# Kernel tuning notes

Hardware: AMD Instinct MI355X
Metric: run time of the kernel (lower is better)

The kernel has to match this reference:

```python
import jax, jax.numpy as jnp
import numpy as np

B, L, D, Q, H = 16, 2048, 1024, 1024, 256
NEG_NUM = -10000.0


def setup_inputs() -> dict:
    key = jax.random.key(0)
    ks = jax.random.split(key, 8)
    ctx = jax.random.normal(ks[0], (B, L, D), dtype=jnp.float32)
    query = jax.random.normal(ks[1], (B, Q), dtype=jnp.float32)
    mask = jax.random.randint(ks[2], (B, L), 0, 2, dtype=jnp.int32)
    # lin_in2proj: Linear(D+Q, H)
    lim1 = 1.0 / np.sqrt(D + Q)
    W1 = jax.random.uniform(ks[3], (H, D + Q), jnp.float32, -lim1, lim1)
    b1 = jax.random.uniform(ks[4], (H,), jnp.float32, -lim1, lim1)
    # lin_proj2score: weight_norm(Linear(H, 1)), dim=0 -> g scalar per row
    lim2 = 1.0 / np.sqrt(H)
    v = jax.random.uniform(ks[5], (1, H), jnp.float32, -lim2, lim2)
    g = jnp.linalg.norm(v).reshape(1, 1)  # weight_norm init: g = ||v||
    b2 = jax.random.uniform(ks[6], (1,), jnp.float32, -lim2, lim2)
    return {"ctx": ctx, "query": query, "mask": mask,
            "W1": W1, "b1": b1, "v": v, "g": g, "b2": b2}


def reference(ctx, query, mask, W1, b1, v, g, b2):
    d = ctx.shape[-1]
    # concat([ctx, query_expanded]) @ W1^T == ctx @ W1c^T + query @ W1q^T
    Wc, Wq = W1[:, :d], W1[:, d:]
    hid = jnp.tanh(jnp.einsum('bld,hd->blh', ctx, Wc)
                   + jnp.einsum('bq,hq->bh', query, Wq)[:, None, :]
                   + b1)                                 # (B, L, H)
    w2 = (g * v / jnp.linalg.norm(v))[0]                 # weight-normed row (H,)
    score = jnp.einsum('blh,h->bl', hid, w2) + b2[0]     # (B, L)
    score = jnp.where(mask == 1, NEG_NUM, score)
    p_ctx = jax.nn.softmax(score, axis=-1)               # (B, L)
    expected_ctx = jnp.einsum('bl,bld->bd', p_ctx, ctx)  # (B, D)
    return expected_ctx, p_ctx
```

## Files before the change

### kernel.cpp

```cpp
#include <hip/hip_runtime.h>
#include <hip/hip_bf16.h>

#define BB 16
#define LCTX 2048
#define DDIM 1024
#define QDIM 1024
#define HDIM 256
#define NEGV -10000.0f

typedef __attribute__((ext_vector_type(8))) short short8;
typedef __attribute__((ext_vector_type(4))) float f32x4;

__device__ inline unsigned short f2bf(float x) {
    unsigned int u = __float_as_uint(x);
    unsigned int r = (u + 0x7fffu + ((u >> 16) & 1u)) >> 16;
    return (unsigned short)r;
}

__global__ __launch_bounds__(256) void k_prep(const float* __restrict__ query,
                                              const float* __restrict__ W1,
                                              const float* __restrict__ b1,
                                              const float* __restrict__ v,
                                              const float* __restrict__ g,
                                              float* __restrict__ qproj,
                                              unsigned short* __restrict__ Wc_sw,
                                              float* __restrict__ w2) {
    int bid = blockIdx.x;
    if (bid < 1024) {
        int b = bid >> 6;
        int hq = bid & 63;
        int wid = threadIdx.x >> 6, lane = threadIdx.x & 63;
        int h = hq * 4 + wid;
        const float* q = query + b * QDIM;
        const float* w = W1 + (size_t)h * (DDIM + QDIM) + DDIM;
        float s = 0.f;
        #pragma unroll 4
        for (int k = lane; k < QDIM; k += 64) s += q[k] * w[k];
        #pragma unroll
        for (int o = 32; o; o >>= 1) s += __shfl_down(s, o);
        if (lane == 0) qproj[b * HDIM + h] = s + b1[h];
    } else if (bid < 1280) {
        int h = bid - 1024;
        const float* src = W1 + (size_t)h * (DDIM + QDIM);
        int hx = h & 7;
        for (int d = threadIdx.x; d < DDIM; d += 256) {
            int kt = d >> 6;
            int s  = (d >> 3) & 7;
            int dl = d & 7;
            int dp = (kt << 6) + ((s ^ hx) << 3) + dl;
            Wc_sw[h * DDIM + dp] = f2bf(src[d]);
        }
    } else {
        __shared__ float red[256];
        float vv = (threadIdx.x < HDIM) ? v[threadIdx.x] : 0.f;
        red[threadIdx.x] = vv * vv;
        __syncthreads();
        for (int o = 128; o; o >>= 1) {
            if (threadIdx.x < o) red[threadIdx.x] += red[threadIdx.x + o];
            __syncthreads();
        }
        float nrm = sqrtf(red[0]);
        if (threadIdx.x < HDIM) w2[threadIdx.x] = g[0] * vv / nrm;
    }
}

__global__ __launch_bounds__(256, 3) void k_score(const float* __restrict__ ctx,
                                                  const unsigned short* __restrict__ Wc_sw,
                                                  const float* __restrict__ qproj,
                                                  const float* __restrict__ w2,
                                                  const float* __restrict__ b2,
                                                  const int* __restrict__ mask,
                                                  float* __restrict__ e_ws,
                                                  float* __restrict__ esum_ws,
                                                  float* __restrict__ part) {
    __shared__ unsigned short At[64 * 64];
    __shared__ unsigned short Wt[256 * 64];
    int tid = threadIdx.x;
    int wid = tid >> 6, lane = tid & 63;
    int hl = lane & 15, lhi = lane >> 4;
    int bid = blockIdx.x;
    int row0 = bid * 64;
    int b = row0 >> 11;

    float qp[4], wv[4];
    #pragma unroll
    for (int ht = 0; ht < 4; ht++) {
        int h = wid * 64 + ht * 16 + hl;
        qp[ht] = qproj[b * HDIM + h];
        wv[ht] = w2[h];
    }

    f32x4 acc[4][4];
    #pragma unroll
    for (int mt = 0; mt < 4; mt++)
        #pragma unroll
        for (int ht = 0; ht < 4; ht++)
            acc[mt][ht] = (f32x4){0.f, 0.f, 0.f, 0.f};

    int srow = tid >> 2;
    int scol = (tid & 3) * 16;
    const float* csrc = ctx + (size_t)(row0 + srow) * DDIM + scol;
    int c0 = (tid & 3) * 2;
    int sx = srow & 7;

    for (int kt = 0; kt < 16; kt++) {
        #pragma unroll
        for (int i = 0; i < 8; i++) {
            int n = i * 256 + tid;
            const unsigned short* gsrc = Wc_sw + (size_t)(n >> 3) * DDIM + kt * 64 + (n & 7) * 8;
            __builtin_amdgcn_global_load_lds(
                (const __attribute__((address_space(1))) unsigned int*)gsrc,
                (__attribute__((address_space(3))) unsigned int*)(Wt + (i * 256 + (tid & ~63)) * 8),
                16, 0, 0);
        }
        const float* cp = csrc + kt * 64;
        float4 cv0 = *(const float4*)(cp + 0);
        float4 cv1 = *(const float4*)(cp + 4);
        float4 cv2 = *(const float4*)(cp + 8);
        float4 cv3 = *(const float4*)(cp + 12);
        short8 p0 = { (short)f2bf(cv0.x), (short)f2bf(cv0.y), (short)f2bf(cv0.z), (short)f2bf(cv0.w),
                      (short)f2bf(cv1.x), (short)f2bf(cv1.y), (short)f2bf(cv1.z), (short)f2bf(cv1.w) };
        short8 p1 = { (short)f2bf(cv2.x), (short)f2bf(cv2.y), (short)f2bf(cv2.z), (short)f2bf(cv2.w),
                      (short)f2bf(cv3.x), (short)f2bf(cv3.y), (short)f2bf(cv3.z), (short)f2bf(cv3.w) };
        *(short8*)(At + srow * 64 + (((c0 + 0) ^ sx) << 3)) = p0;
        *(short8*)(At + srow * 64 + (((c0 + 1) ^ sx) << 3)) = p1;
        __syncthreads();

        #pragma unroll
        for (int ks = 0; ks < 2; ks++) {
            int s = ks * 4 + lhi;
            short8 af[4], bfr[4];
            #pragma unroll
            for (int mt = 0; mt < 4; mt++) {
                int m = mt * 16 + hl;
                af[mt] = *(const short8*)(At + m * 64 + ((s ^ (m & 7)) << 3));
            }
            #pragma unroll
            for (int ht = 0; ht < 4; ht++) {
                int h = wid * 64 + ht * 16 + hl;
                bfr[ht] = *(const short8*)(Wt + h * 64 + ((s ^ (h & 7)) << 3));
            }
            #pragma unroll
            for (int mt = 0; mt < 4; mt++)
                #pragma unroll
                for (int ht = 0; ht < 4; ht++)
                    acc[mt][ht] = __builtin_amdgcn_mfma_f32_16x16x32_bf16(af[mt], bfr[ht], acc[mt][ht], 0, 0, 0);
        }
        __syncthreads();
    }

    float* sb  = (float*)At;
    float* sbe = sb + 256;
    #pragma unroll
    for (int mt = 0; mt < 4; mt++) {
        #pragma unroll
        for (int r = 0; r < 4; r++) {
            float partial = 0.f;
            #pragma unroll
            for (int ht = 0; ht < 4; ht++) {
                float x = acc[mt][ht][r] + qp[ht];
                x = fminf(fmaxf(x, -15.f), 15.f);
                float e = __expf(2.f * x);
                partial += (e - 1.f) / (e + 1.f) * wv[ht];
            }
            #pragma unroll
            for (int o = 1; o < 16; o <<= 1) partial += __shfl_xor(partial, o);
            if (hl == 0) sb[wid * 64 + mt * 16 + lhi * 4 + r] = partial;
        }
    }
    __syncthreads();

    if (tid < 64) {
        float s = sb[tid] + sb[64 + tid] + sb[128 + tid] + sb[192 + tid] + b2[0];
        int grow = row0 + tid;
        int bb = grow >> 11, ll = grow & 2047;
        float e = (mask[bb * 2048 + ll] == 1) ? 0.f : __expf(s);
        e_ws[grow] = e;
        sbe[tid] = e;
        float tot = e;
        #pragma unroll
        for (int o = 32; o; o >>= 1) tot += __shfl_down(tot, o);
        if (tid == 0) esum_ws[bid] = tot;
    }
    __syncthreads();

    {
        int d0 = tid * 4;
        const float* cb = ctx + (size_t)row0 * DDIM + d0;
        float4 a = {0.f, 0.f, 0.f, 0.f};
        #pragma unroll 8
        for (int l = 0; l < 64; l++) {
            float el = sbe[l];
            float4 c = *(const float4*)(cb + (size_t)l * DDIM);
            a.x += el * c.x; a.y += el * c.y; a.z += el * c.z; a.w += el * c.w;
        }
        *(float4*)(part + (size_t)bid * DDIM + d0) = a;
    }
}

__global__ __launch_bounds__(256) void k_norm(const float* __restrict__ e_ws,
                                              const float* __restrict__ esum_ws,
                                              const float* __restrict__ part,
                                              float* __restrict__ out_exp,
                                              float* __restrict__ out_p) {
    int b = blockIdx.x, dc = blockIdx.y;
    int tid = threadIdx.x;
    float se = 0.f;
    #pragma unroll
    for (int j = 0; j < 32; j++) se += esum_ws[b * 32 + j];
    float inv = 1.f / se;
    if (tid < 128) {
        int d = dc * 128 + tid;
        float s = 0.f;
        #pragma unroll
        for (int j = 0; j < 32; j++) s += part[(size_t)(b * 32 + j) * DDIM + d];
        out_exp[b * DDIM + d] = s * inv;
    }
    int l = dc * 256 + tid;
    out_p[b * LCTX + l] = e_ws[b * LCTX + l] * inv;
}

extern "C" void kernel_launch(void* const* d_in, const int* in_sizes, int n_in,
                              void* d_out, int out_size, void* d_ws, size_t ws_size,
                              hipStream_t stream) {
    const float* ctx   = (const float*)d_in[0];
    const float* query = (const float*)d_in[1];
    const int*   mask  = (const int*)d_in[2];
    const float* W1    = (const float*)d_in[3];
    const float* b1    = (const float*)d_in[4];
    const float* v     = (const float*)d_in[5];
    const float* g     = (const float*)d_in[6];
    const float* b2    = (const float*)d_in[7];
    float* out_exp = (float*)d_out;
    float* out_p   = (float*)d_out + 16384;

    char* ws = (char*)d_ws;
    unsigned short* Wc_sw = (unsigned short*)ws;
    float* qproj = (float*)(ws + 524288);
    float* w2    = (float*)(ws + 540672);
    float* e_ws  = (float*)(ws + 541696);
    float* esum  = (float*)(ws + 672768);
    float* part  = (float*)(ws + 674816);

    k_prep <<<dim3(1281),   256, 0, stream>>>(query, W1, b1, v, g, qproj, Wc_sw, w2);
    k_score<<<dim3(512),    256, 0, stream>>>(ctx, Wc_sw, qproj, w2, b2, mask, e_ws, esum, part);
    k_norm <<<dim3(16, 8),  256, 0, stream>>>(e_ws, esum, part, out_exp, out_p);
}
```

Baseline: 59.15 us.

## Double-buffer W and ctx tiles with manual waitcnt software pipeline in k_score

Measured after the change: 59.87 us. Within noise of the previous version (+1.2%).

```diff
diff --git a/kernel.cpp b/kernel.cpp
--- a/kernel.cpp
+++ b/kernel.cpp
@@ -64,7 +64,7 @@
     }
 }
 
-__global__ __launch_bounds__(256, 3) void k_score(const float* __restrict__ ctx,
+__global__ __launch_bounds__(256, 2) void k_score(const float* __restrict__ ctx,
                                                   const unsigned short* __restrict__ Wc_sw,
                                                   const float* __restrict__ qproj,
                                                   const float* __restrict__ w2,
@@ -73,82 +73,125 @@
                                                   float* __restrict__ e_ws,
                                                   float* __restrict__ esum_ws,
                                                   float* __restrict__ part) {
-    __shared__ unsigned short At[64 * 64];
-    __shared__ unsigned short Wt[256 * 64];
+    __shared__ unsigned short Wt[2][256 * 64];
+    __shared__ unsigned short At[2][64 * 64];
     int tid = threadIdx.x;
     int wid = tid >> 6, lane = tid & 63;
     int hl = lane & 15, lhi = lane >> 4;
     int bid = blockIdx.x;
     int row0 = bid * 64;
     int b = row0 >> 11;
+    int wrow0 = wid * 64;
+
+    f32x4 acc[4][4];
+    #pragma unroll
+    for (int mt = 0; mt < 4; mt++)
+        #pragma unroll
+        for (int ht = 0; ht < 4; ht++)
+            acc[mt][ht] = (f32x4){0.f, 0.f, 0.f, 0.f};
+
+    int srow = tid >> 2;
+    int c0 = (tid & 3) * 2;
+    int sx = srow & 7;
+    const float* csrc = ctx + (size_t)(row0 + srow) * DDIM + (tid & 3) * 16;
+
+    float4 a0, a1, a2, a3, b0, b1, b2v, b3;
+
+#define STAGE_W(BUF, KT) do { \
+    _Pragma("unroll") \
+    for (int i_ = 0; i_ < 8; i_++) { \
+        const unsigned short* gsrc_ = Wc_sw + (size_t)(wrow0 + i_ * 8 + (lane >> 3)) * DDIM + (KT) * 64 + (lane & 7) * 8; \
+        __builtin_amdgcn_global_load_lds( \
+            (const __attribute__((address_space(1))) unsigned int*)gsrc_, \
+            (__attribute__((address_space(3))) unsigned int*)(&Wt[BUF][(wrow0 + i_ * 8) * 64]), \
+            16, 0, 0); \
+    } } while (0)
+
+#define CTX_ISSUE(KT, R0, R1, R2, R3) do { \
+    const float* cp_ = csrc + (KT) * 64; \
+    R0 = *(const float4*)(cp_ + 0);  R1 = *(const float4*)(cp_ + 4); \
+    R2 = *(const float4*)(cp_ + 8);  R3 = *(const float4*)(cp_ + 12); } while (0)
+
+#define WRITE_A(BUF, U0, U1, U2, U3) do { \
+    short8 p0_ = { (short)f2bf(U0.x), (short)f2bf(U0.y), (short)f2bf(U0.z), (short)f2bf(U0.w), \
+                   (short)f2bf(U1.x), (short)f2bf(U1.y), (short)f2bf(U1.z), (short)f2bf(U1.w) }; \
+    short8 p1_ = { (short)f2bf(U2.x), (short)f2bf(U2.y), (short)f2bf(U2.z), (short)f2bf(U2.w), \
+                   (short)f2bf(U3.x), (short)f2bf(U3.y), (short)f2bf(U3.z), (short)f2bf(U3.w) }; \
+    *(short8*)(&At[BUF][srow * 64 + (((c0 + 0) ^ sx) << 3)]) = p0_; \
+    *(short8*)(&At[BUF][srow * 64 + (((c0 + 1) ^ sx) << 3)]) = p1_; } while (0)
+
+#define COMPUTE(BUF) do { \
+    __builtin_amdgcn_s_setprio(1); \
+    _Pragma("unroll") \
+    for (int ks_ = 0; ks_ < 2; ks_++) { \
+        int s_ = ks_ * 4 + lhi; \
+        int xc_ = (s_ ^ (hl & 7)) << 3; \
+        short8 af_[4], bf_[4]; \
+        _Pragma("unroll") \
+        for (int mt_ = 0; mt_ < 4; mt_++) \
+            af_[mt_] = *(const short8*)(&At[BUF][(mt_ * 16 + hl) * 64 + xc_]); \
+        _Pragma("unroll") \
+        for (int ht_ = 0; ht_ < 4; ht_++) \
+            bf_[ht_] = *(const short8*)(&Wt[BUF][(wrow0 + ht_ * 16 + hl) * 64 + xc_]); \
+        _Pragma("unroll") \
+        for (int mt_ = 0; mt_ < 4; mt_++) \
+            _Pragma("unroll") \
+            for (int ht_ = 0; ht_ < 4; ht_++) \
+                acc[mt_][ht_] = __builtin_amdgcn_mfma_f32_16x16x32_bf16(af_[mt_], bf_[ht_], acc[mt_][ht_], 0, 0, 0); \
+    } \
+    __builtin_amdgcn_s_setprio(0); } while (0)
+
+#define BODY(T, R0, R1, R2, R3, U0, U1, U2, U3) do { \
+    STAGE_W(((T) + 1) & 1, ((T) + 1) & 15); \
+    __builtin_amdgcn_sched_barrier(0); \
+    CTX_ISSUE(((T) + 2) & 15, R0, R1, R2, R3); \
+    __builtin_amdgcn_sched_barrier(0); \
+    asm volatile("s_waitcnt vmcnt(16)" ::: "memory"); \
+    __builtin_amdgcn_sched_barrier(0); \
+    COMPUTE((T) & 1); \
+    asm volatile("s_waitcnt vmcnt(12)" ::: "memory"); \
+    __builtin_amdgcn_sched_barrier(0); \
+    WRITE_A(((T) + 1) & 1, U0, U1, U2, U3); \
+    asm volatile("s_waitcnt lgkmcnt(0)" ::: "memory"); \
+    __builtin_amdgcn_s_barrier(); \
+    __builtin_amdgcn_sched_barrier(0); } while (0)
+
+    CTX_ISSUE(0, a0, a1, a2, a3);
+    __builtin_amdgcn_sched_barrier(0);
+    STAGE_W(0, 0);
+    __builtin_amdgcn_sched_barrier(0);
+    asm volatile("s_waitcnt vmcnt(8)" ::: "memory");
+    __builtin_amdgcn_sched_barrier(0);
+    WRITE_A(0, a0, a1, a2, a3);
+    CTX_ISSUE(1, b0, b1, b2v, b3);
+    asm volatile("s_waitcnt lgkmcnt(0)" ::: "memory");
+    __builtin_amdgcn_s_barrier();
+    __builtin_amdgcn_sched_barrier(0);
+
+    BODY(0,  a0, a1, a2, a3,  b0, b1, b2v, b3);
+    BODY(1,  b0, b1, b2v, b3, a0, a1, a2, a3);
+    BODY(2,  a0, a1, a2, a3,  b0, b1, b2v, b3);
+    BODY(3,  b0, b1, b2v, b3, a0, a1, a2, a3);
+    BODY(4,  a0, a1, a2, a3,  b0, b1, b2v, b3);
+    BODY(5,  b0, b1, b2v, b3, a0, a1, a2, a3);
+    BODY(6,  a0, a1, a2, a3,  b0, b1, b2v, b3);
+    BODY(7,  b0, b1, b2v, b3, a0, a1, a2, a3);
+    BODY(8,  a0, a1, a2, a3,  b0, b1, b2v, b3);
+    BODY(9,  b0, b1, b2v, b3, a0, a1, a2, a3);
+    BODY(10, a0, a1, a2, a3,  b0, b1, b2v, b3);
+    BODY(11, b0, b1, b2v, b3, a0, a1, a2, a3);
+    BODY(12, a0, a1, a2, a3,  b0, b1, b2v, b3);
+    BODY(13, b0, b1, b2v, b3, a0, a1, a2, a3);
+    BODY(14, a0, a1, a2, a3,  b0, b1, b2v, b3);
+    BODY(15, b0, b1, b2v, b3, a0, a1, a2, a3);
 
     float qp[4], wv[4];
     #pragma unroll
     for (int ht = 0; ht < 4; ht++) {
-        int h = wid * 64 + ht * 16 + hl;
+        int h = wrow0 + ht * 16 + hl;
         qp[ht] = qproj[b * HDIM + h];
         wv[ht] = w2[h];
     }
-
-    f32x4 acc[4][4];
-    #pragma unroll
-    for (int mt = 0; mt < 4; mt++)
-        #pragma unroll
-        for (int ht = 0; ht < 4; ht++)
-            acc[mt][ht] = (f32x4){0.f, 0.f, 0.f, 0.f};
-
-    int srow = tid >> 2;
-    int scol = (tid & 3) * 16;
-    const float* csrc = ctx + (size_t)(row0 + srow) * DDIM + scol;
-    int c0 = (tid & 3) * 2;
-    int sx = srow & 7;
-
-    for (int kt = 0; kt < 16; kt++) {
-        #pragma unroll
-        for (int i = 0; i < 8; i++) {
-            int n = i * 256 + tid;
-            const unsigned short* gsrc = Wc_sw + (size_t)(n >> 3) * DDIM + kt * 64 + (n & 7) * 8;
-            __builtin_amdgcn_global_load_lds(
-                (const __attribute__((address_space(1))) unsigned int*)gsrc,
-                (__attribute__((address_space(3))) unsigned int*)(Wt + (i * 256 + (tid & ~63)) * 8),
-                16, 0, 0);
-        }
-        const float* cp = csrc + kt * 64;
-        float4 cv0 = *(const float4*)(cp + 0);
-        float4 cv1 = *(const float4*)(cp + 4);
-        float4 cv2 = *(const float4*)(cp + 8);
-        float4 cv3 = *(const float4*)(cp + 12);
-        short8 p0 = { (short)f2bf(cv0.x), (short)f2bf(cv0.y), (short)f2bf(cv0.z), (short)f2bf(cv0.w),
-                      (short)f2bf(cv1.x), (short)f2bf(cv1.y), (short)f2bf(cv1.z), (short)f2bf(cv1.w) };
-        short8 p1 = { (short)f2bf(cv2.x), (short)f2bf(cv2.y), (short)f2bf(cv2.z), (short)f2bf(cv2.w),
-                      (short)f2bf(cv3.x), (short)f2bf(cv3.y), (short)f2bf(cv3.z), (short)f2bf(cv3.w) };
-        *(short8*)(At + srow * 64 + (((c0 + 0) ^ sx) << 3)) = p0;
-        *(short8*)(At + srow * 64 + (((c0 + 1) ^ sx) << 3)) = p1;
-        __syncthreads();
-
-        #pragma unroll
-        for (int ks = 0; ks < 2; ks++) {
-            int s = ks * 4 + lhi;
-            short8 af[4], bfr[4];
-            #pragma unroll
-            for (int mt = 0; mt < 4; mt++) {
-                int m = mt * 16 + hl;
-                af[mt] = *(const short8*)(At + m * 64 + ((s ^ (m & 7)) << 3));
-            }
-            #pragma unroll
-            for (int ht = 0; ht < 4; ht++) {
-                int h = wid * 64 + ht * 16 + hl;
-                bfr[ht] = *(const short8*)(Wt + h * 64 + ((s ^ (h & 7)) << 3));
-            }
-            #pragma unroll
-            for (int mt = 0; mt < 4; mt++)
-                #pragma unroll
-                for (int ht = 0; ht < 4; ht++)
-                    acc[mt][ht] = __builtin_amdgcn_mfma_f32_16x16x32_bf16(af[mt], bfr[ht], acc[mt][ht], 0, 0, 0);
-        }
-        __syncthreads();
-    }
-
     float* sb  = (float*)At;
     float* sbe = sb + 256;
     #pragma unroll
@@ -191,8 +234,8 @@
         #pragma unroll 8
         for (int l = 0; l < 64; l++) {
             float el = sbe[l];
-            float4 c = *(const float4*)(cb + (size_t)l * DDIM);
-            a.x += el * c.x; a.y += el * c.y; a.z += el * c.z; a.w += el * c.w;
+            float4 cc = *(const float4*)(cb + (size_t)l * DDIM);
+            a.x += el * cc.x; a.y += el * cc.y; a.z += el * cc.z; a.w += el * cc.w;
         }
         *(float4*)(part + (size_t)bid * DDIM + d0) = a;
     }
```

## Double-buffer ctx staging, read weights from global, split weighted sum into kernel

Applied to the files above, without the earlier changes.

New measurement: 90.73 us. +53.4%, slower.

```diff
diff --git a/kernel.cpp b/kernel.cpp
--- a/kernel.cpp
+++ b/kernel.cpp
@@ -6,7 +6,6 @@
 #define DDIM 1024
 #define QDIM 1024
 #define HDIM 256
-#define NEGV -10000.0f
 
 typedef __attribute__((ext_vector_type(8))) short short8;
 typedef __attribute__((ext_vector_type(4))) float f32x4;
@@ -23,7 +22,7 @@
                                               const float* __restrict__ v,
                                               const float* __restrict__ g,
                                               float* __restrict__ qproj,
-                                              unsigned short* __restrict__ Wc_sw,
+                                              unsigned short* __restrict__ Wc_kmaj,
                                               float* __restrict__ w2) {
     int bid = blockIdx.x;
     if (bid < 1024) {
@@ -42,13 +41,11 @@
     } else if (bid < 1280) {
         int h = bid - 1024;
         const float* src = W1 + (size_t)h * (DDIM + QDIM);
-        int hx = h & 7;
         for (int d = threadIdx.x; d < DDIM; d += 256) {
             int kt = d >> 6;
-            int s  = (d >> 3) & 7;
-            int dl = d & 7;
-            int dp = (kt << 6) + ((s ^ hx) << 3) + dl;
-            Wc_sw[h * DDIM + dp] = f2bf(src[d]);
+            int oct = (d >> 3) & 7;
+            int j = d & 7;
+            Wc_kmaj[(size_t)kt * 16384 + h * 64 + oct * 8 + j] = f2bf(src[d]);
         }
     } else {
         __shared__ float red[256];
@@ -64,23 +61,83 @@
     }
 }
 
-__global__ __launch_bounds__(256, 3) void k_score(const float* __restrict__ ctx,
-                                                  const unsigned short* __restrict__ Wc_sw,
+__global__ __launch_bounds__(256, 2) void k_score(const float* __restrict__ ctx,
+                                                  const unsigned short* __restrict__ Wc_kmaj,
                                                   const float* __restrict__ qproj,
                                                   const float* __restrict__ w2,
-                                                  const float* __restrict__ b2,
+                                                  const float* __restrict__ b2p,
                                                   const int* __restrict__ mask,
                                                   float* __restrict__ e_ws,
-                                                  float* __restrict__ esum_ws,
-                                                  float* __restrict__ part) {
-    __shared__ unsigned short At[64 * 64];
-    __shared__ unsigned short Wt[256 * 64];
+                                                  float* __restrict__ esum_ws) {
+    __shared__ unsigned short At[2][64 * 256];
     int tid = threadIdx.x;
     int wid = tid >> 6, lane = tid & 63;
     int hl = lane & 15, lhi = lane >> 4;
-    int bid = blockIdx.x;
-    int row0 = bid * 64;
+    int row0 = blockIdx.x * 64;
     int b = row0 >> 11;
+
+    f32x4 acc[4][4];
+    #pragma unroll
+    for (int mt = 0; mt < 4; mt++)
+        #pragma unroll
+        for (int ht = 0; ht < 4; ht++)
+            acc[mt][ht] = (f32x4){0.f, 0.f, 0.f, 0.f};
+
+    int srow = tid >> 2;
+    int q = tid & 3;
+    int sxr = srow & 7;
+    const float* csrc = ctx + (size_t)(row0 + srow) * DDIM + q * 64;
+
+#define STAGE(BUF, G) do { \
+    const float* sp_ = csrc + (G) * 256; \
+    _Pragma("unroll") \
+    for (int bat_ = 0; bat_ < 4; bat_++) { \
+        float4 v0_ = *(const float4*)(sp_ + bat_ * 16 + 0); \
+        float4 v1_ = *(const float4*)(sp_ + bat_ * 16 + 4); \
+        float4 v2_ = *(const float4*)(sp_ + bat_ * 16 + 8); \
+        float4 v3_ = *(const float4*)(sp_ + bat_ * 16 + 12); \
+        short8 h0_ = { (short)f2bf(v0_.x), (short)f2bf(v0_.y), (short)f2bf(v0_.z), (short)f2bf(v0_.w), \
+                       (short)f2bf(v1_.x), (short)f2bf(v1_.y), (short)f2bf(v1_.z), (short)f2bf(v1_.w) }; \
+        short8 h1_ = { (short)f2bf(v2_.x), (short)f2bf(v2_.y), (short)f2bf(v2_.z), (short)f2bf(v2_.w), \
+                       (short)f2bf(v3_.x), (short)f2bf(v3_.y), (short)f2bf(v3_.z), (short)f2bf(v3_.w) }; \
+        int o0_ = (q * 8 + bat_ * 2 + 0) ^ sxr; \
+        int o1_ = (q * 8 + bat_ * 2 + 1) ^ sxr; \
+        *(short8*)(&At[BUF][srow * 256 + o0_ * 8]) = h0_; \
+        *(short8*)(&At[BUF][srow * 256 + o1_ * 8]) = h1_; \
+    } } while (0)
+
+#define COMPUTE(BUF, G) do { \
+    _Pragma("unroll") \
+    for (int kt_ = 0; kt_ < 4; kt_++) { \
+        int ktg_ = (G) * 4 + kt_; \
+        _Pragma("unroll") \
+        for (int ks_ = 0; ks_ < 2; ks_++) { \
+            int sl_ = kt_ * 8 + ks_ * 4 + lhi; \
+            short8 af_[4], bf_[4]; \
+            _Pragma("unroll") \
+            for (int mt_ = 0; mt_ < 4; mt_++) { \
+                int m_ = mt_ * 16 + hl; \
+                af_[mt_] = *(const short8*)(&At[BUF][m_ * 256 + (sl_ ^ (m_ & 7)) * 8]); \
+            } \
+            _Pragma("unroll") \
+            for (int ht_ = 0; ht_ < 4; ht_++) { \
+                int h_ = wid * 64 + ht_ * 16 + hl; \
+                bf_[ht_] = *(const short8*)(Wc_kmaj + (size_t)ktg_ * 16384 + h_ * 64 + (ks_ * 4 + lhi) * 8); \
+            } \
+            _Pragma("unroll") \
+            for (int mt_ = 0; mt_ < 4; mt_++) \
+                _Pragma("unroll") \
+                for (int ht_ = 0; ht_ < 4; ht_++) \
+                    acc[mt_][ht_] = __builtin_amdgcn_mfma_f32_16x16x32_bf16(af_[mt_], bf_[ht_], acc[mt_][ht_], 0, 0, 0); \
+        } } } while (0)
+
+    STAGE(0, 0);
+    __syncthreads();
+    COMPUTE(0, 0); STAGE(1, 1); __syncthreads();
+    COMPUTE(1, 1); STAGE(0, 2); __syncthreads();
+    COMPUTE(0, 2); STAGE(1, 3); __syncthreads();
+    COMPUTE(1, 3);
+    __syncthreads();
 
     float qp[4], wv[4];
     #pragma unroll
@@ -89,66 +146,6 @@
         qp[ht] = qproj[b * HDIM + h];
         wv[ht] = w2[h];
     }
-
-    f32x4 acc[4][4];
-    #pragma unroll
-    for (int mt = 0; mt < 4; mt++)
-        #pragma unroll
-        for (int ht = 0; ht < 4; ht++)
-            acc[mt][ht] = (f32x4){0.f, 0.f, 0.f, 0.f};
-
-    int srow = tid >> 2;
-    int scol = (tid & 3) * 16;
-    const float* csrc = ctx + (size_t)(row0 + srow) * DDIM + scol;
-    int c0 = (tid & 3) * 2;
-    int sx = srow & 7;
-
-    for (int kt = 0; kt < 16; kt++) {
-        #pragma unroll
-        for (int i = 0; i < 8; i++) {
-            int n = i * 256 + tid;
-            const unsigned short* gsrc = Wc_sw + (size_t)(n >> 3) * DDIM + kt * 64 + (n & 7) * 8;
-            __builtin_amdgcn_global_load_lds(
-                (const __attribute__((address_space(1))) unsigned int*)gsrc,
-                (__attribute__((address_space(3))) unsigned int*)(Wt + (i * 256 + (tid & ~63)) * 8),
-                16, 0, 0);
-        }
-        const float* cp = csrc + kt * 64;
-        float4 cv0 = *(const float4*)(cp + 0);
-        float4 cv1 = *(const float4*)(cp + 4);
-        float4 cv2 = *(const float4*)(cp + 8);
-        float4 cv3 = *(const float4*)(cp + 12);
-        short8 p0 = { (short)f2bf(cv0.x), (short)f2bf(cv0.y), (short)f2bf(cv0.z), (short)f2bf(cv0.w),
-                      (short)f2bf(cv1.x), (short)f2bf(cv1.y), (short)f2bf(cv1.z), (short)f2bf(cv1.w) };
-        short8 p1 = { (short)f2bf(cv2.x), (short)f2bf(cv2.y), (short)f2bf(cv2.z), (short)f2bf(cv2.w),
-                      (short)f2bf(cv3.x), (short)f2bf(cv3.y), (short)f2bf(cv3.z), (short)f2bf(cv3.w) };
-        *(short8*)(At + srow * 64 + (((c0 + 0) ^ sx) << 3)) = p0;
-        *(short8*)(At + srow * 64 + (((c0 + 1) ^ sx) << 3)) = p1;
-        __syncthreads();
-
-        #pragma unroll
-        for (int ks = 0; ks < 2; ks++) {
-            int s = ks * 4 + lhi;
-            short8 af[4], bfr[4];
-            #pragma unroll
-            for (int mt = 0; mt < 4; mt++) {
-                int m = mt * 16 + hl;
-                af[mt] = *(const short8*)(At + m * 64 + ((s ^ (m & 7)) << 3));
-            }
-            #pragma unroll
-            for (int ht = 0; ht < 4; ht++) {
-                int h = wid * 64 + ht * 16 + hl;
-                bfr[ht] = *(const short8*)(Wt + h * 64 + ((s ^ (h & 7)) << 3));
-            }
-            #pragma unroll
-            for (int mt = 0; mt < 4; mt++)
-                #pragma unroll
-                for (int ht = 0; ht < 4; ht++)
-                    acc[mt][ht] = __builtin_amdgcn_mfma_f32_16x16x32_bf16(af[mt], bfr[ht], acc[mt][ht], 0, 0, 0);
-        }
-        __syncthreads();
-    }
-
     float* sb  = (float*)At;
     float* sbe = sb + 256;
     #pragma unroll
@@ -160,8 +157,8 @@
             for (int ht = 0; ht < 4; ht++) {
                 float x = acc[mt][ht][r] + qp[ht];
                 x = fminf(fmaxf(x, -15.f), 15.f);
-                float e = __expf(2.f * x);
-                partial += (e - 1.f) / (e + 1.f) * wv[ht];
+                float e2 = __expf(2.f * x);
+                partial += (e2 - 1.f) / (e2 + 1.f) * wv[ht];
             }
             #pragma unroll
             for (int o = 1; o < 16; o <<= 1) partial += __shfl_xor(partial, o);
@@ -171,31 +168,48 @@
     __syncthreads();
 
     if (tid < 64) {
-        float s = sb[tid] + sb[64 + tid] + sb[128 + tid] + sb[192 + tid] + b2[0];
+        float s = sb[tid] + sb[64 + tid] + sb[128 + tid] + sb[192 + tid] + b2p[0];
         int grow = row0 + tid;
-        int bb = grow >> 11, ll = grow & 2047;
-        float e = (mask[bb * 2048 + ll] == 1) ? 0.f : __expf(s);
+        float e = (mask[b * 2048 + (grow & 2047)] == 1) ? 0.f : __expf(s);
         e_ws[grow] = e;
         sbe[tid] = e;
         float tot = e;
         #pragma unroll
         for (int o = 32; o; o >>= 1) tot += __shfl_down(tot, o);
-        if (tid == 0) esum_ws[bid] = tot;
-    }
-    __syncthreads();
-
-    {
-        int d0 = tid * 4;
-        const float* cb = ctx + (size_t)row0 * DDIM + d0;
-        float4 a = {0.f, 0.f, 0.f, 0.f};
-        #pragma unroll 8
-        for (int l = 0; l < 64; l++) {
-            float el = sbe[l];
-            float4 c = *(const float4*)(cb + (size_t)l * DDIM);
-            a.x += el * c.x; a.y += el * c.y; a.z += el * c.z; a.w += el * c.w;
-        }
-        *(float4*)(part + (size_t)bid * DDIM + d0) = a;
-    }
+        if (tid == 0) esum_ws[blockIdx.x] = tot;
+    }
+}
+
+__global__ __launch_bounds__(256) void k_exp(const float* __restrict__ ctx,
+                                             const float* __restrict__ e_ws,
+                                             float* __restrict__ part) {
+    int b = blockIdx.x, ls = blockIdx.y;
+    int wid = threadIdx.x >> 6, lane = threadIdx.x & 63;
+    __shared__ float red[4][1024];
+
+    f32x4 a0 = {0,0,0,0}, a1 = {0,0,0,0}, a2 = {0,0,0,0}, a3 = {0,0,0,0};
+    const float* base = ctx + ((size_t)b * LCTX + ls * 64 + wid * 16) * DDIM + lane * 16;
+    const float* ep = e_ws + b * LCTX + ls * 64 + wid * 16;
+
+    #pragma unroll 4
+    for (int i = 0; i < 16; i++) {
+        float e = ep[i];
+        const f32x4* p = (const f32x4*)(base + (size_t)i * DDIM);
+        f32x4 v0 = p[0], v1 = p[1], v2 = p[2], v3 = p[3];
+        a0 += e * v0; a1 += e * v1; a2 += e * v2; a3 += e * v3;
+    }
+    *(f32x4*)(&red[wid][lane * 16 + 0])  = a0;
+    *(f32x4*)(&red[wid][lane * 16 + 4])  = a1;
+    *(f32x4*)(&red[wid][lane * 16 + 8])  = a2;
+    *(f32x4*)(&red[wid][lane * 16 + 12]) = a3;
+    __syncthreads();
+
+    int d0 = threadIdx.x * 4;
+    f32x4 s = *(const f32x4*)(&red[0][d0]);
+    s += *(const f32x4*)(&red[1][d0]);
+    s += *(const f32x4*)(&red[2][d0]);
+    s += *(const f32x4*)(&red[3][d0]);
+    *(f32x4*)(part + ((size_t)(b * 32 + ls)) * DDIM + d0) = s;
 }
 
 __global__ __launch_bounds__(256) void k_norm(const float* __restrict__ e_ws,
@@ -235,14 +249,15 @@
     float* out_p   = (float*)d_out + 16384;
 
     char* ws = (char*)d_ws;
-    unsigned short* Wc_sw = (unsigned short*)ws;
+    unsigned short* Wc_kmaj = (unsigned short*)ws;
     float* qproj = (float*)(ws + 524288);
     float* w2    = (float*)(ws + 540672);
     float* e_ws  = (float*)(ws + 541696);
     float* esum  = (float*)(ws + 672768);
     float* part  = (float*)(ws + 674816);
 
-    k_prep <<<dim3(1281),   256, 0, stream>>>(query, W1, b1, v, g, qproj, Wc_sw, w2);
-    k_score<<<dim3(512),    256, 0, stream>>>(ctx, Wc_sw, qproj, w2, b2, mask, e_ws, esum, part);
-    k_norm <<<dim3(16, 8),  256, 0, stream>>>(e_ws, esum, part, out_exp, out_p);
-}
+    k_prep <<<dim3(1281),    256, 0, stream>>>(query, W1, b1, v, g, qproj, Wc_kmaj, w2);
+    k_score<<<dim3(512),     256, 0, stream>>>(ctx, Wc_kmaj, qproj, w2, b2, mask, e_ws, esum);
+    k_exp  <<<dim3(16, 32),  256, 0, stream>>>(ctx, e_ws, part);
+    k_norm <<<dim3(16, 8),   256, 0, stream>>>(e_ws, esum, part, out_exp, out_p);
+}
```

## Split expected-context weighted sum out of score kernel into separate kernel

Applied to the files above, without the earlier changes.

New measurement: 70.07 us. 18.5% more time.

```diff
diff --git a/kernel.cpp b/kernel.cpp
--- a/kernel.cpp
+++ b/kernel.cpp
@@ -6,7 +6,6 @@
 #define DDIM 1024
 #define QDIM 1024
 #define HDIM 256
-#define NEGV -10000.0f
 
 typedef __attribute__((ext_vector_type(8))) short short8;
 typedef __attribute__((ext_vector_type(4))) float f32x4;
@@ -68,11 +67,10 @@
                                                   const unsigned short* __restrict__ Wc_sw,
                                                   const float* __restrict__ qproj,
                                                   const float* __restrict__ w2,
-                                                  const float* __restrict__ b2,
+                                                  const float* __restrict__ b2p,
                                                   const int* __restrict__ mask,
                                                   float* __restrict__ e_ws,
-                                                  float* __restrict__ esum_ws,
-                                                  float* __restrict__ part) {
+                                                  float* __restrict__ esum_ws) {
     __shared__ unsigned short At[64 * 64];
     __shared__ unsigned short Wt[256 * 64];
     int tid = threadIdx.x;
@@ -98,10 +96,9 @@
             acc[mt][ht] = (f32x4){0.f, 0.f, 0.f, 0.f};
 
     int srow = tid >> 2;
-    int scol = (tid & 3) * 16;
-    const float* csrc = ctx + (size_t)(row0 + srow) * DDIM + scol;
     int c0 = (tid & 3) * 2;
     int sx = srow & 7;
+    const float* csrc = ctx + (size_t)(row0 + srow) * DDIM + (tid & 3) * 16;
 
     for (int kt = 0; kt < 16; kt++) {
         #pragma unroll
@@ -150,7 +147,6 @@
     }
 
     float* sb  = (float*)At;
-    float* sbe = sb + 256;
     #pragma unroll
     for (int mt = 0; mt < 4; mt++) {
         #pragma unroll
@@ -160,8 +156,8 @@
             for (int ht = 0; ht < 4; ht++) {
                 float x = acc[mt][ht][r] + qp[ht];
                 x = fminf(fmaxf(x, -15.f), 15.f);
-                float e = __expf(2.f * x);
-                partial += (e - 1.f) / (e + 1.f) * wv[ht];
+                float e2 = __expf(2.f * x);
+                partial += (e2 - 1.f) / (e2 + 1.f) * wv[ht];
             }
             #pragma unroll
             for (int o = 1; o < 16; o <<= 1) partial += __shfl_xor(partial, o);
@@ -171,31 +167,47 @@
     __syncthreads();
 
     if (tid < 64) {
-        float s = sb[tid] + sb[64 + tid] + sb[128 + tid] + sb[192 + tid] + b2[0];
+        float s = sb[tid] + sb[64 + tid] + sb[128 + tid] + sb[192 + tid] + b2p[0];
         int grow = row0 + tid;
-        int bb = grow >> 11, ll = grow & 2047;
-        float e = (mask[bb * 2048 + ll] == 1) ? 0.f : __expf(s);
+        float e = (mask[b * 2048 + (grow & 2047)] == 1) ? 0.f : __expf(s);
         e_ws[grow] = e;
-        sbe[tid] = e;
         float tot = e;
         #pragma unroll
         for (int o = 32; o; o >>= 1) tot += __shfl_down(tot, o);
         if (tid == 0) esum_ws[bid] = tot;
     }
+}
+
+__global__ __launch_bounds__(256) void k_exp(const float* __restrict__ ctx,
+                                             const float* __restrict__ e_ws,
+                                             float* __restrict__ part) {
+    int b = blockIdx.x, ls = blockIdx.y;
+    int wid = threadIdx.x >> 6, lane = threadIdx.x & 63;
+    __shared__ float red[4][1024];
+
+    f32x4 a0 = {0,0,0,0}, a1 = {0,0,0,0}, a2 = {0,0,0,0}, a3 = {0,0,0,0};
+    const float* base = ctx + ((size_t)b * LCTX + ls * 64 + wid * 16) * DDIM + lane * 16;
+    const float* ep = e_ws + b * LCTX + ls * 64 + wid * 16;
+
+    #pragma unroll 4
+    for (int i = 0; i < 16; i++) {
+        float e = ep[i];
+        const f32x4* p = (const f32x4*)(base + (size_t)i * DDIM);
+        f32x4 v0 = p[0], v1 = p[1], v2 = p[2], v3 = p[3];
+        a0 += e * v0; a1 += e * v1; a2 += e * v2; a3 += e * v3;
+    }
+    *(f32x4*)(&red[wid][lane * 16 + 0])  = a0;
+    *(f32x4*)(&red[wid][lane * 16 + 4])  = a1;
+    *(f32x4*)(&red[wid][lane * 16 + 8])  = a2;
+    *(f32x4*)(&red[wid][lane * 16 + 12]) = a3;
     __syncthreads();
 
-    {
-        int d0 = tid * 4;
-        const float* cb = ctx + (size_t)row0 * DDIM + d0;
-        float4 a = {0.f, 0.f, 0.f, 0.f};
-        #pragma unroll 8
-        for (int l = 0; l < 64; l++) {
-            float el = sbe[l];
-            float4 c = *(const float4*)(cb + (size_t)l * DDIM);
-            a.x += el * c.x; a.y += el * c.y; a.z += el * c.z; a.w += el * c.w;
-        }
-        *(float4*)(part + (size_t)bid * DDIM + d0) = a;
-    }
+    int d0 = threadIdx.x * 4;
+    f32x4 s = *(const f32x4*)(&red[0][d0]);
+    s += *(const f32x4*)(&red[1][d0]);
+    s += *(const f32x4*)(&red[2][d0]);
+    s += *(const f32x4*)(&red[3][d0]);
+    *(f32x4*)(part + ((size_t)(b * 32 + ls)) * DDIM + d0) = s;
 }
 
 __global__ __launch_bounds__(256) void k_norm(const float* __restrict__ e_ws,
@@ -242,7 +254,8 @@
     float* esum  = (float*)(ws + 672768);
     float* part  = (float*)(ws + 674816);
 
-    k_prep <<<dim3(1281),   256, 0, stream>>>(query, W1, b1, v, g, qproj, Wc_sw, w2);
-    k_score<<<dim3(512),    256, 0, stream>>>(ctx, Wc_sw, qproj, w2, b2, mask, e_ws, esum, part);
-    k_norm <<<dim3(16, 8),  256, 0, stream>>>(e_ws, esum, part, out_exp, out_p);
-}
+    k_prep <<<dim3(1281),    256, 0, stream>>>(query, W1, b1, v, g, qproj, Wc_sw, w2);
+    k_score<<<dim3(512),     256, 0, stream>>>(ctx, Wc_sw, qproj, w2, b2, mask, e_ws, esum);
+    k_exp  <<<dim3(16, 32),  256, 0, stream>>>(ctx, e_ws, part);
+    k_norm <<<dim3(16, 8),   256, 0, stream>>>(e_ws, esum, part, out_exp, out_p);
+}
```
